# Optimization experiments

Hardware: AMD Instinct MI355X
Metric: run time of the kernel (lower is better)

The kernel has to match this reference:

```python
import jax, jax.numpy as jnp
import numpy as np

NUM_CLASSES = 20   # M = len(unique(true)); label 0 is background (skipped)
ALPHA = 0.7
BETA = 1.5


def setup_inputs() -> dict:
    key = jax.random.key(0)
    k1, k2, k3 = jax.random.split(key, 3)
    B, N, K = 1, 262144, 128
    points = jax.random.normal(k1, (B, N, 3), dtype=jnp.float32)
    true = jax.random.randint(k2, (B, N), 0, NUM_CLASSES)
    embedding = jax.random.normal(k3, (B, N, K), dtype=jnp.float32)
    return {"points": points, "true": true, "embedding": embedding}


def reference(points, true, embedding):
    # points: (B,N,3), true: (B,N) int labels in [0,M), embedding: (B,N,K). B == 1.
    B, N, K = embedding.shape
    M = NUM_CLASSES
    t = true[0]  # (N,)

    # g = sigmoid(||p||) per point
    g = jax.nn.sigmoid(jnp.sqrt(jnp.sum(points ** 2, axis=-1)))  # (B,N)

    # per-cluster counts and embedding means (segment reduce over N)
    counts = jax.ops.segment_sum(jnp.ones((N,), points.dtype), t, num_segments=M)  # (M,)
    safe_counts = jnp.maximum(counts, 1.0)
    means = jax.ops.segment_sum(embedding[0], t, num_segments=M) / safe_counts[:, None]  # (M,K)

    # intra-cluster: per point, distance to its cluster mean
    d = jnp.sqrt(jnp.sum((embedding - means[true]) ** 2, axis=-1))  # (B,N)
    per_point = g * jnp.square(jnp.maximum(d - ALPHA, 0.0))         # (B,N)
    intra_per_cluster = jax.ops.segment_sum(per_point[0], t, num_segments=M) / safe_counts  # (M,)
    intra = jnp.sum(intra_per_cluster[1:])  # sum over clusters 1..M-1 (skip background 0)

    # inter-cluster: pairwise mean distances among foreground clusters
    me = means[1:]                                    # (M-1, K)
    sq = jnp.sum((me[:, None, :] - me[None, :, :]) ** 2, axis=-1)  # (M-1, M-1)
    eye = jnp.eye(M - 1, dtype=sq.dtype)
    dist = jnp.sqrt(jnp.where(eye > 0, 1.0, sq))      # safe sqrt on diagonal
    inter = jnp.sum((1.0 - eye) * jnp.square(jnp.maximum(BETA - dist, 0.0)))

    return jnp.broadcast_to(intra / M + inter / (M * (M - 1)), (B,))
```

## Files before the change

kernel.cpp:

```cpp
#include <hip/hip_runtime.h>
#include <hip/hip_bf16.h>
#include <math.h>

#define NCLS 20
#define KDIM 128
#define ALPHA 0.7f
#define BETA 1.5f

#define WS_SUMS 0
#define WS_INTRA 2560
#define WS_CUR 2580
#define WS_ZERO_N 2600
#define WS_BKT 4096

#define GRID 2048
#define SUMS_GRID 1027

__global__ void k_init(float* ws) {
    const int tid = threadIdx.x;
    for (int i = tid; i < WS_ZERO_N; i += 256) ws[i] = 0.0f;
}

__global__ void __launch_bounds__(256) k_scatter(const int* __restrict__ t,
                                                 float* __restrict__ ws, int N) {
    __shared__ int ih[NCLS], lbase[NCLS];
    const int tid = threadIdx.x;
    if (tid < NCLS) ih[tid] = 0;
    __syncthreads();
    const int g = blockIdx.x * 256 + tid;
    int c = -1, r = 0;
    if (g < N) {
        c = t[g];
        r = atomicAdd(&ih[c], 1);
    }
    __syncthreads();
    if (tid < NCLS && ih[tid]) lbase[tid] = atomicAdd((int*)&ws[WS_CUR] + tid, ih[tid]);
    __syncthreads();
    if (c >= 0) {
        int* bkt = (int*)&ws[WS_BKT];
        bkt[(size_t)c * N + lbase[c] + r] = g;
    }
}

__global__ void __launch_bounds__(256) k_sums(const float4* __restrict__ emb4,
                                              float* __restrict__ ws, int N) {
    __shared__ float lsum[NCLS * KDIM];
    const int tid = threadIdx.x;
    for (int i = tid; i < NCLS * KDIM; i += 256) lsum[i] = 0.0f;
    __syncthreads();

    const int s = tid & 31;
    const int u = blockIdx.x * 8 + (tid >> 5);
    const int* gc = (const int*)&ws[WS_CUR];

    int cls = -1, off = 0, m = 0;
    {
        int cum = 0;
#pragma unroll
        for (int c = 0; c < NCLS; c++) {
            const int cnt = gc[c];
            const int v = (cnt + 31) >> 5;
            if (u >= cum && u < cum + v) {
                cls = c;
                off = (u - cum) * 32;
                m = min(32, cnt - off);
            }
            cum += v;
        }
    }

    if (cls >= 0) {
        const int* bkt = (const int*)&ws[WS_BKT] + (size_t)cls * N + off;
        const int bidx = bkt[min(s, m - 1)];
        float4 acc = make_float4(0.f, 0.f, 0.f, 0.f);
        if (m == 32) {
#pragma unroll
            for (int j0 = 0; j0 < 32; j0 += 8) {
                float4 v0, v1, v2, v3, v4, v5, v6, v7;
#define G(jj) { const int idx = __shfl(bidx, j0 + jj, 32);  \
                v##jj = emb4[(size_t)idx * 32 + s]; }
                G(0) G(1) G(2) G(3) G(4) G(5) G(6) G(7)
#undef G
                acc.x += v0.x + v1.x + v2.x + v3.x + v4.x + v5.x + v6.x + v7.x;
                acc.y += v0.y + v1.y + v2.y + v3.y + v4.y + v5.y + v6.y + v7.y;
                acc.z += v0.z + v1.z + v2.z + v3.z + v4.z + v5.z + v6.z + v7.z;
                acc.w += v0.w + v1.w + v2.w + v3.w + v4.w + v5.w + v6.w + v7.w;
            }
        } else {
            for (int j = 0; j < m; j++) {
                const int idx = __shfl(bidx, j, 32);
                const float4 v = emb4[(size_t)idx * 32 + s];
                acc.x += v.x; acc.y += v.y; acc.z += v.z; acc.w += v.w;
            }
        }
        float* a = &lsum[cls * KDIM + 4 * s];
        unsafeAtomicAdd(a + 0, acc.x);
        unsafeAtomicAdd(a + 1, acc.y);
        unsafeAtomicAdd(a + 2, acc.z);
        unsafeAtomicAdd(a + 3, acc.w);
    }
    __syncthreads();

    for (int i = tid; i < NCLS * KDIM; i += 256)
        if (lsum[i] != 0.0f) unsafeAtomicAdd(&ws[WS_SUMS + i], lsum[i]);
}

__global__ void __launch_bounds__(256) k_intra(const float4* __restrict__ emb4,
                                               const int* __restrict__ t,
                                               const float* __restrict__ pts,
                                               float* __restrict__ ws, int N) {
    __shared__ float lmean[NCLS * KDIM];
    __shared__ float lintra[NCLS];
    const int tid = threadIdx.x;
    const int* gc = (const int*)&ws[WS_CUR];
    for (int i = tid; i < NCLS * KDIM; i += 256) {
        const float cnt = (float)gc[i / KDIM];
        lmean[i] = ws[WS_SUMS + i] / fmaxf(cnt, 1.0f);
    }
    if (tid < NCLS) lintra[tid] = 0.0f;
    __syncthreads();

    const int s = tid & 31;
    const int pp = tid >> 5;
    const int stride = GRID * 8;
    for (int p = blockIdx.x * 8 + pp; p < N; p += 2 * stride) {
        const int p1 = p + stride;
        {
            const int c = t[p];
            const float4 v = emb4[(size_t)p * 32 + s];
            const float4 mm = *(const float4*)&lmean[c * KDIM + 4 * s];
            float dx = v.x - mm.x, dy = v.y - mm.y, dz = v.z - mm.z, dw = v.w - mm.w;
            float d2 = dx * dx + dy * dy + dz * dz + dw * dw;
            for (int off = 16; off >= 1; off >>= 1) d2 += __shfl_down(d2, off, 32);
            if (s == 0) {
                const float d = sqrtf(d2);
                const float px = pts[(size_t)p * 3 + 0];
                const float py = pts[(size_t)p * 3 + 1];
                const float pz = pts[(size_t)p * 3 + 2];
                const float r = sqrtf(px * px + py * py + pz * pz);
                const float g = 1.0f / (1.0f + expf(-r));
                const float h = fmaxf(d - ALPHA, 0.0f);
                unsafeAtomicAdd(&lintra[c], g * h * h);
            }
        }
        if (p1 < N) {
            const int c = t[p1];
            const float4 v = emb4[(size_t)p1 * 32 + s];
            const float4 mm = *(const float4*)&lmean[c * KDIM + 4 * s];
            float dx = v.x - mm.x, dy = v.y - mm.y, dz = v.z - mm.z, dw = v.w - mm.w;
            float d2 = dx * dx + dy * dy + dz * dz + dw * dw;
            for (int off = 16; off >= 1; off >>= 1) d2 += __shfl_down(d2, off, 32);
            if (s == 0) {
                const float d = sqrtf(d2);
                const float px = pts[(size_t)p1 * 3 + 0];
                const float py = pts[(size_t)p1 * 3 + 1];
                const float pz = pts[(size_t)p1 * 3 + 2];
                const float r = sqrtf(px * px + py * py + pz * pz);
                const float g = 1.0f / (1.0f + expf(-r));
                const float h = fmaxf(d - ALPHA, 0.0f);
                unsafeAtomicAdd(&lintra[c], g * h * h);
            }
        }
    }
    __syncthreads();
    if (tid < NCLS) unsafeAtomicAdd(&ws[WS_INTRA + tid], lintra[tid]);
}

__global__ void __launch_bounds__(256) k_final(const float* __restrict__ ws,
                                               float* __restrict__ out) {
    __shared__ float lmean[NCLS * KDIM];
    __shared__ float red[256];
    const int tid = threadIdx.x;
    const int* gc = (const int*)&ws[WS_CUR];
    for (int i = tid; i < NCLS * KDIM; i += 256) {
        const float cnt = (float)gc[i / KDIM];
        lmean[i] = ws[WS_SUMS + i] / fmaxf(cnt, 1.0f);
    }
    __syncthreads();

    float acc = 0.0f;
    for (int idx = tid; idx < 361; idx += 256) {
        const int i = idx / 19 + 1;
        const int j = idx % 19 + 1;
        if (i != j) {
            float sq = 0.0f;
            const float* mi = lmean + i * KDIM;
            const float* mj = lmean + j * KDIM;
            for (int k = 0; k < KDIM; k++) {
                const float df = mi[k] - mj[k];
                sq += df * df;
            }
            const float dist = sqrtf(sq);
            const float h = fmaxf(BETA - dist, 0.0f);
            acc += h * h;
        }
    }
    red[tid] = acc;
    __syncthreads();
    for (int st = 128; st >= 1; st >>= 1) {
        if (tid < st) red[tid] += red[tid + st];
        __syncthreads();
    }
    if (tid == 0) {
        float intra = 0.0f;
        for (int c = 1; c < NCLS; c++)
            intra += ws[WS_INTRA + c] / fmaxf((float)gc[c], 1.0f);
        out[0] = intra / (float)NCLS + red[0] / (float)(NCLS * (NCLS - 1));
    }
}

#define FB_BLK 128
#define FB_GRID 2048
#define FBW_SUMS 0
#define FBW_CNT 2560
#define FBW_INTRA 2580
__global__ void __launch_bounds__(256) k_init_fb(float* ws) {
    const int tid = threadIdx.x;
    for (int i = tid; i < 2600; i += 256) ws[i] = 0.0f;
}
__global__ void __launch_bounds__(FB_BLK) k_sums_fb(const float4* __restrict__ emb4,
                                                    const int* __restrict__ t,
                                                    float* ws, int N) {
    __shared__ float lsum[2][NCLS * KDIM];
    __shared__ float lcnt[NCLS];
    __shared__ int lds_t[FB_BLK];
    const int tid = threadIdx.x;
    const int w = tid >> 6, k = tid & 63;
    const int half = k >> 5;
    const int k31 = k & 31;
    for (int i = tid; i < 2 * NCLS * KDIM; i += FB_BLK) (&lsum[0][0])[i] = 0.0f;
    if (tid < NCLS) lcnt[tid] = 0.0f;
    __syncthreads();
    const int chunk = blockIdx.x * FB_BLK;
    const int npts = min(FB_BLK, N - chunk);
    if (tid < npts) {
        const int c = t[chunk + tid];
        lds_t[tid] = c;
        unsafeAtomicAdd(&lcnt[c], 1.0f);
    }
    __syncthreads();
    float* L = lsum[w];
    for (int q = 32 * w; q < 32 * w + 32; q++) {
        const int pl = 2 * q + half;
        if (pl < npts) {
            const int c = lds_t[pl];
            const float4 v = emb4[(size_t)(chunk + pl) * 32 + k31];
            const int cA = __shfl(c, 0, 64);
            const int cB = __shfl(c, 32, 64);
            if (cA == cB) {
                float4 vv;
                vv.x = v.x + __shfl_xor(v.x, 32, 64);
                vv.y = v.y + __shfl_xor(v.y, 32, 64);
                vv.z = v.z + __shfl_xor(v.z, 32, 64);
                vv.w = v.w + __shfl_xor(v.w, 32, 64);
                if (half == 0) {
                    float4* a = (float4*)&L[cA * KDIM + 4 * k31];
                    float4 o = *a;
                    o.x += vv.x; o.y += vv.y; o.z += vv.z; o.w += vv.w;
                    *a = o;
                }
            } else {
                float4* a = (float4*)&L[c * KDIM + 4 * k31];
                float4 o = *a;
                o.x += v.x; o.y += v.y; o.z += v.z; o.w += v.w;
                *a = o;
            }
        }
    }
    __syncthreads();
    for (int i = tid; i < NCLS * KDIM; i += FB_BLK)
        unsafeAtomicAdd(&ws[FBW_SUMS + i], lsum[0][i] + lsum[1][i]);
    if (tid < NCLS) unsafeAtomicAdd(&ws[FBW_CNT + tid], lcnt[tid]);
}
__global__ void __launch_bounds__(256) k_intra_fb(const float4* __restrict__ emb4,
                                                  const int* __restrict__ t,
                                                  const float* __restrict__ pts,
                                                  float* ws, int N) {
    __shared__ float lmean[NCLS * KDIM];
    __shared__ float lintra[NCLS];
    const int tid = threadIdx.x;
    for (int i = tid; i < NCLS * KDIM; i += 256)
        lmean[i] = ws[FBW_SUMS + i] / fmaxf(ws[FBW_CNT + i / KDIM], 1.0f);
    if (tid < NCLS) lintra[tid] = 0.0f;
    __syncthreads();
    const int s = tid & 31;
    const int pp = tid >> 5;
    const int stride = FB_GRID * 8;
    for (int p = blockIdx.x * 8 + pp; p < N; p += stride) {
        const int c = t[p];
        const float4 v = emb4[(size_t)p * 32 + s];
        const float4 mm = *(const float4*)&lmean[c * KDIM + 4 * s];
        float dx = v.x - mm.x, dy = v.y - mm.y, dz = v.z - mm.z, dw = v.w - mm.w;
        float d2 = dx * dx + dy * dy + dz * dz + dw * dw;
        for (int off = 16; off >= 1; off >>= 1) d2 += __shfl_down(d2, off, 32);
        if (s == 0) {
            const float d = sqrtf(d2);
            const float px = pts[(size_t)p * 3 + 0];
            const float py = pts[(size_t)p * 3 + 1];
            const float pz = pts[(size_t)p * 3 + 2];
            const float r = sqrtf(px * px + py * py + pz * pz);
            const float g = 1.0f / (1.0f + expf(-r));
            const float h = fmaxf(d - ALPHA, 0.0f);
            unsafeAtomicAdd(&lintra[c], g * h * h);
        }
    }
    __syncthreads();
    if (tid < NCLS) unsafeAtomicAdd(&ws[FBW_INTRA + tid], lintra[tid]);
}
__global__ void __launch_bounds__(256) k_final_fb(const float* ws, float* out) {
    __shared__ float lmean[NCLS * KDIM];
    __shared__ float red[256];
    const int tid = threadIdx.x;
    for (int i = tid; i < NCLS * KDIM; i += 256)
        lmean[i] = ws[FBW_SUMS + i] / fmaxf(ws[FBW_CNT + i / KDIM], 1.0f);
    __syncthreads();
    float acc = 0.0f;
    for (int idx = tid; idx < 361; idx += 256) {
        const int i = idx / 19 + 1;
        const int j = idx % 19 + 1;
        if (i != j) {
            float sq = 0.0f;
            const float* mi = lmean + i * KDIM;
            const float* mj = lmean + j * KDIM;
            for (int k = 0; k < KDIM; k++) {
                const float df = mi[k] - mj[k];
                sq += df * df;
            }
            const float dist = sqrtf(sq);
            const float h = fmaxf(BETA - dist, 0.0f);
            acc += h * h;
        }
    }
    red[tid] = acc;
    __syncthreads();
    for (int st = 128; st >= 1; st >>= 1) {
        if (tid < st) red[tid] += red[tid + st];
        __syncthreads();
    }
    if (tid == 0) {
        float intra = 0.0f;
        for (int c = 1; c < NCLS; c++)
            intra += ws[FBW_INTRA + c] / fmaxf(ws[FBW_CNT + c], 1.0f);
        out[0] = intra / (float)NCLS + red[0] / (float)(NCLS * (NCLS - 1));
    }
}

extern "C" void kernel_launch(void* const* d_in, const int* in_sizes, int n_in,
                              void* d_out, int out_size, void* d_ws, size_t ws_size,
                              hipStream_t stream) {
    const float* pts = (const float*)d_in[0];
    const int* t = (const int*)d_in[1];
    const float4* emb4 = (const float4*)d_in[2];
    float* out = (float*)d_out;
    float* ws = (float*)d_ws;
    const int N = in_sizes[1];
    const size_t need = ((size_t)WS_BKT + (size_t)NCLS * (size_t)N) * 4;

    if (ws_size >= need) {
        k_init<<<1, 256, 0, stream>>>(ws);
        k_scatter<<<(N + 255) / 256, 256, 0, stream>>>(t, ws, N);
        k_sums<<<SUMS_GRID, 256, 0, stream>>>(emb4, ws, N);
        k_intra<<<GRID, 256, 0, stream>>>(emb4, t, pts, ws, N);
        k_final<<<1, 256, 0, stream>>>(ws, out);
    } else {
        k_init_fb<<<1, 256, 0, stream>>>(ws);
        k_sums_fb<<<FB_GRID, FB_BLK, 0, stream>>>(emb4, t, ws, N);
        k_intra_fb<<<FB_GRID, 256, 0, stream>>>(emb4, t, pts, ws, N);
        k_final_fb<<<1, 256, 0, stream>>>(ws, out);
    }
}
```

Measured before the change: 110.8 us.

## Iterate intra pass over class buckets and precompute sigmoid weights in scatter

```diff
diff --git a/kernel.cpp b/kernel.cpp
--- a/kernel.cpp
+++ b/kernel.cpp
@@ -11,7 +11,7 @@
 #define WS_INTRA 2560
 #define WS_CUR 2580
 #define WS_ZERO_N 2600
-#define WS_BKT 4096
+#define WS_G 4096
 
 #define GRID 2048
 #define SUMS_GRID 1027
@@ -22,27 +22,49 @@
 }
 
 __global__ void __launch_bounds__(256) k_scatter(const int* __restrict__ t,
-                                                 float* __restrict__ ws, int N) {
+                                                 const float* __restrict__ pts,
+                                                 float* __restrict__ ws,
+                                                 float* __restrict__ g,
+                                                 int* __restrict__ bkt, int N) {
     __shared__ int ih[NCLS], lbase[NCLS];
     const int tid = threadIdx.x;
     if (tid < NCLS) ih[tid] = 0;
     __syncthreads();
-    const int g = blockIdx.x * 256 + tid;
+    const int gid = blockIdx.x * 256 + tid;
     int c = -1, r = 0;
-    if (g < N) {
-        c = t[g];
+    if (gid < N) {
+        c = t[gid];
         r = atomicAdd(&ih[c], 1);
+        const float px = pts[(size_t)gid * 3 + 0];
+        const float py = pts[(size_t)gid * 3 + 1];
+        const float pz = pts[(size_t)gid * 3 + 2];
+        const float rad = sqrtf(px * px + py * py + pz * pz);
+        g[gid] = 1.0f / (1.0f + expf(-rad));
     }
     __syncthreads();
     if (tid < NCLS && ih[tid]) lbase[tid] = atomicAdd((int*)&ws[WS_CUR] + tid, ih[tid]);
     __syncthreads();
-    if (c >= 0) {
-        int* bkt = (int*)&ws[WS_BKT];
-        bkt[(size_t)c * N + lbase[c] + r] = g;
+    if (c >= 0) bkt[(size_t)c * N + lbase[c] + r] = gid;
+}
+
+__device__ inline void hw_map(const int* gc, int u, int& cls, int& off, int& m) {
+    cls = -1; off = 0; m = 0;
+    int cum = 0;
+#pragma unroll
+    for (int c = 0; c < NCLS; c++) {
+        const int cnt = gc[c];
+        const int v = (cnt + 31) >> 5;
+        if (u >= cum && u < cum + v) {
+            cls = c;
+            off = (u - cum) * 32;
+            m = min(32, cnt - off);
+        }
+        cum += v;
     }
 }
 
 __global__ void __launch_bounds__(256) k_sums(const float4* __restrict__ emb4,
+                                              const int* __restrict__ bkt,
                                               float* __restrict__ ws, int N) {
     __shared__ float lsum[NCLS * KDIM];
     const int tid = threadIdx.x;
@@ -51,27 +73,12 @@
 
     const int s = tid & 31;
     const int u = blockIdx.x * 8 + (tid >> 5);
-    const int* gc = (const int*)&ws[WS_CUR];
-
-    int cls = -1, off = 0, m = 0;
-    {
-        int cum = 0;
-#pragma unroll
-        for (int c = 0; c < NCLS; c++) {
-            const int cnt = gc[c];
-            const int v = (cnt + 31) >> 5;
-            if (u >= cum && u < cum + v) {
-                cls = c;
-                off = (u - cum) * 32;
-                m = min(32, cnt - off);
-            }
-            cum += v;
-        }
-    }
+    int cls, off, m;
+    hw_map((const int*)&ws[WS_CUR], u, cls, off, m);
 
     if (cls >= 0) {
-        const int* bkt = (const int*)&ws[WS_BKT] + (size_t)cls * N + off;
-        const int bidx = bkt[min(s, m - 1)];
+        const int* b = bkt + (size_t)cls * N + off;
+        const int bidx = b[min(s, m - 1)];
         float4 acc = make_float4(0.f, 0.f, 0.f, 0.f);
         if (m == 32) {
 #pragma unroll
@@ -106,61 +113,67 @@
 }
 
 __global__ void __launch_bounds__(256) k_intra(const float4* __restrict__ emb4,
-                                               const int* __restrict__ t,
-                                               const float* __restrict__ pts,
+                                               const float* __restrict__ g,
+                                               const int* __restrict__ bkt,
                                                float* __restrict__ ws, int N) {
     __shared__ float lmean[NCLS * KDIM];
     __shared__ float lintra[NCLS];
     const int tid = threadIdx.x;
     const int* gc = (const int*)&ws[WS_CUR];
-    for (int i = tid; i < NCLS * KDIM; i += 256) {
-        const float cnt = (float)gc[i / KDIM];
-        lmean[i] = ws[WS_SUMS + i] / fmaxf(cnt, 1.0f);
-    }
+    for (int i = tid; i < NCLS * KDIM; i += 256)
+        lmean[i] = ws[WS_SUMS + i] / fmaxf((float)gc[i / KDIM], 1.0f);
     if (tid < NCLS) lintra[tid] = 0.0f;
     __syncthreads();
 
     const int s = tid & 31;
-    const int pp = tid >> 5;
-    const int stride = GRID * 8;
-    for (int p = blockIdx.x * 8 + pp; p < N; p += 2 * stride) {
-        const int p1 = p + stride;
-        {
-            const int c = t[p];
-            const float4 v = emb4[(size_t)p * 32 + s];
-            const float4 mm = *(const float4*)&lmean[c * KDIM + 4 * s];
-            float dx = v.x - mm.x, dy = v.y - mm.y, dz = v.z - mm.z, dw = v.w - mm.w;
-            float d2 = dx * dx + dy * dy + dz * dz + dw * dw;
-            for (int off = 16; off >= 1; off >>= 1) d2 += __shfl_down(d2, off, 32);
-            if (s == 0) {
-                const float d = sqrtf(d2);
-                const float px = pts[(size_t)p * 3 + 0];
-                const float py = pts[(size_t)p * 3 + 1];
-                const float pz = pts[(size_t)p * 3 + 2];
-                const float r = sqrtf(px * px + py * py + pz * pz);
-                const float g = 1.0f / (1.0f + expf(-r));
-                const float h = fmaxf(d - ALPHA, 0.0f);
-                unsafeAtomicAdd(&lintra[c], g * h * h);
-            }
-        }
-        if (p1 < N) {
-            const int c = t[p1];
-            const float4 v = emb4[(size_t)p1 * 32 + s];
-            const float4 mm = *(const float4*)&lmean[c * KDIM + 4 * s];
-            float dx = v.x - mm.x, dy = v.y - mm.y, dz = v.z - mm.z, dw = v.w - mm.w;
-            float d2 = dx * dx + dy * dy + dz * dz + dw * dw;
-            for (int off = 16; off >= 1; off >>= 1) d2 += __shfl_down(d2, off, 32);
-            if (s == 0) {
-                const float d = sqrtf(d2);
-                const float px = pts[(size_t)p1 * 3 + 0];
-                const float py = pts[(size_t)p1 * 3 + 1];
-                const float pz = pts[(size_t)p1 * 3 + 2];
-                const float r = sqrtf(px * px + py * py + pz * pz);
-                const float g = 1.0f / (1.0f + expf(-r));
-                const float h = fmaxf(d - ALPHA, 0.0f);
-                unsafeAtomicAdd(&lintra[c], g * h * h);
-            }
-        }
+    const int u = blockIdx.x * 8 + (tid >> 5);
+    int cls, off, m;
+    hw_map(gc, u, cls, off, m);
+
+    if (cls >= 0) {
+        const float4 mr = *(const float4*)&lmean[cls * KDIM + 4 * s];
+        const int* b = bkt + (size_t)cls * N + off;
+        const int bidx = b[min(s, m - 1)];
+        float part = 0.f;
+        if (m == 32) {
+#pragma unroll
+            for (int j0 = 0; j0 < 32; j0 += 8) {
+                float4 v0, v1, v2, v3, v4, v5, v6, v7;
+                int i0, i1, i2, i3, i4, i5, i6, i7;
+#define G(jj) { i##jj = __shfl(bidx, j0 + jj, 32);          \
+                v##jj = emb4[(size_t)i##jj * 32 + s]; }
+                G(0) G(1) G(2) G(3) G(4) G(5) G(6) G(7)
+#undef G
+#define P(jj) {                                                           \
+    float dx = v##jj.x - mr.x, dy = v##jj.y - mr.y;                       \
+    float dz = v##jj.z - mr.z, dw = v##jj.w - mr.w;                       \
+    float d2 = dx * dx + dy * dy + dz * dz + dw * dw;                     \
+    for (int o = 16; o >= 1; o >>= 1) d2 += __shfl_down(d2, o, 32);       \
+    if (s == 0) {                                                         \
+        const float d = sqrtf(d2);                                        \
+        const float h = fmaxf(d - ALPHA, 0.0f);                           \
+        part = fmaf(g[i##jj], h * h, part);                               \
+    }                                                                     \
+}
+                P(0) P(1) P(2) P(3) P(4) P(5) P(6) P(7)
+#undef P
+            }
+        } else {
+            for (int j = 0; j < m; j++) {
+                const int idx = __shfl(bidx, j, 32);
+                const float4 v = emb4[(size_t)idx * 32 + s];
+                float dx = v.x - mr.x, dy = v.y - mr.y;
+                float dz = v.z - mr.z, dw = v.w - mr.w;
+                float d2 = dx * dx + dy * dy + dz * dz + dw * dw;
+                for (int o = 16; o >= 1; o >>= 1) d2 += __shfl_down(d2, o, 32);
+                if (s == 0) {
+                    const float d = sqrtf(d2);
+                    const float h = fmaxf(d - ALPHA, 0.0f);
+                    part = fmaf(g[idx], h * h, part);
+                }
+            }
+        }
+        if (s == 0 && part != 0.0f) unsafeAtomicAdd(&lintra[cls], part);
     }
     __syncthreads();
     if (tid < NCLS) unsafeAtomicAdd(&ws[WS_INTRA + tid], lintra[tid]);
@@ -172,10 +185,8 @@
     __shared__ float red[256];
     const int tid = threadIdx.x;
     const int* gc = (const int*)&ws[WS_CUR];
-    for (int i = tid; i < NCLS * KDIM; i += 256) {
-        const float cnt = (float)gc[i / KDIM];
-        lmean[i] = ws[WS_SUMS + i] / fmaxf(cnt, 1.0f);
-    }
+    for (int i = tid; i < NCLS * KDIM; i += 256)
+        lmean[i] = ws[WS_SUMS + i] / fmaxf((float)gc[i / KDIM], 1.0f);
     __syncthreads();
 
     float acc = 0.0f;
@@ -299,9 +310,9 @@
             const float py = pts[(size_t)p * 3 + 1];
             const float pz = pts[(size_t)p * 3 + 2];
             const float r = sqrtf(px * px + py * py + pz * pz);
-            const float g = 1.0f / (1.0f + expf(-r));
+            const float gg = 1.0f / (1.0f + expf(-r));
             const float h = fmaxf(d - ALPHA, 0.0f);
-            unsafeAtomicAdd(&lintra[c], g * h * h);
+            unsafeAtomicAdd(&lintra[c], gg * h * h);
         }
     }
     __syncthreads();
@@ -354,13 +365,15 @@
     float* out = (float*)d_out;
     float* ws = (float*)d_ws;
     const int N = in_sizes[1];
-    const size_t need = ((size_t)WS_BKT + (size_t)NCLS * (size_t)N) * 4;
+    float* g = ws + WS_G;
+    int* bkt = (int*)(g + N);
+    const size_t need = ((size_t)WS_G + (size_t)N + (size_t)NCLS * (size_t)N) * 4;
 
     if (ws_size >= need) {
         k_init<<<1, 256, 0, stream>>>(ws);
-        k_scatter<<<(N + 255) / 256, 256, 0, stream>>>(t, ws, N);
-        k_sums<<<SUMS_GRID, 256, 0, stream>>>(emb4, ws, N);
-        k_intra<<<GRID, 256, 0, stream>>>(emb4, t, pts, ws, N);
+        k_scatter<<<(N + 255) / 256, 256, 0, stream>>>(t, pts, ws, g, bkt, N);
+        k_sums<<<SUMS_GRID, 256, 0, stream>>>(emb4, bkt, ws, N);
+        k_intra<<<SUMS_GRID, 256, 0, stream>>>(emb4, g, bkt, ws, N);
         k_final<<<1, 256, 0, stream>>>(ws, out);
     } else {
         k_init_fb<<<1, 256, 0, stream>>>(ws);
```

Measured after the change: 114.9 us. +3.7%, slower.
